# Performance work log

Hardware: AMD Instinct MI355X
Metric: run time of the kernel (lower is better)

Reference implementation:

```python
import jax, jax.numpy as jnp
import numpy as np

N = 4096
S_DIM = 64
A_DIM = 32
HID = 128
HEADS = 4
F = HID // HEADS  # per-head out_features = 32
ALPHA = 0.2       # leaky relu slope
NEG = -9e15       # mask value from the torch code


def _xavier(k, shape, gain=1.0):
    fan_in, fan_out = shape[-2], shape[-1]
    lim = gain * np.sqrt(6.0 / (fan_in + fan_out))
    return jax.random.uniform(k, shape, jnp.float32, -lim, lim)


def setup_inputs() -> dict:
    key = jax.random.key(0)
    ks = jax.random.split(key, 18)
    return {
        "state": jax.random.normal(ks[0], (N, S_DIM), jnp.float32),
        "adj_matrix": jax.random.randint(ks[1], (N, N), 0, 2, jnp.int32),
        # feature extraction MLP
        "W1": _xavier(ks[2], (S_DIM, HID)), "b1": jnp.zeros((HID,), jnp.float32),
        "W2": _xavier(ks[3], (HID, HID)), "b2": jnp.zeros((HID,), jnp.float32),
        # per-head GAT params (stacked over heads); gain=1.414 as in torch init
        "Wg": _xavier(ks[4], (HEADS, HID, F), gain=1.414),
        "ag": _xavier(ks[5], (HEADS, 2 * F, 1), gain=1.414)[..., 0],  # (HEADS, 2F)
        # policy head
        "Wp1": _xavier(ks[6], (HID, HID)), "bp1": jnp.zeros((HID,), jnp.float32),
        "Wp2": _xavier(ks[7], (HID, A_DIM)), "bp2": jnp.zeros((A_DIM,), jnp.float32),
        # value head
        "Wv1": _xavier(ks[8], (HID, HID)), "bv1": jnp.zeros((HID,), jnp.float32),
        "Wv2": _xavier(ks[9], (HID, 1)), "bv2": jnp.zeros((1,), jnp.float32),
    }


def reference(state, adj_matrix, W1, b1, W2, b2, Wg, ag,
              Wp1, bp1, Wp2, bp2, Wv1, bv1, Wv2, bv2):
    # feature extraction MLP: [N, S_DIM] -> [N, HID]
    x = jax.nn.relu(state @ W1 + b1)
    x = jax.nn.relu(x @ W2 + b2)

    # GAT heads (vectorized over heads). h: [H, N, F]
    h = jnp.einsum('nd,hdf->hnf', x, Wg)
    # a^T [h_i || h_j] = a1.h_i + a2.h_j  -> avoid the O(N^2 * 2F) concat
    a1, a2 = ag[:, :F], ag[:, F:]
    s1 = jnp.einsum('hnf,hf->hn', h, a1)  # [H, N]
    s2 = jnp.einsum('hnf,hf->hn', h, a2)  # [H, N]
    e = jax.nn.leaky_relu(s1[:, :, None] + s2[:, None, :], ALPHA)  # [H, N, N]
    mask = adj_matrix > 0
    e = jnp.where(mask[None], e, NEG)
    attn = jax.nn.softmax(e, axis=-1)  # dropout is identity in eval mode
    out = jnp.einsum('hnm,hmf->hnf', attn, h)  # [H, N, F]
    feat = jnp.transpose(out, (1, 0, 2)).reshape(N, HID)  # concat heads along dim=1

    logits = jax.nn.relu(feat @ Wp1 + bp1) @ Wp2 + bp2
    action_probs = jax.nn.softmax(logits, axis=-1)
    state_value = jax.nn.relu(feat @ Wv1 + bv1) @ Wv2 + bv2
    return action_probs, state_value
```

## Files before the change

kernel.cpp:

```cpp
#include <hip/hip_runtime.h>
#include <hip/hip_bf16.h>
#include <hip/hip_fp16.h>

#define NN 4096
#define SDIM 64
#define HID 128
#define HEADS 4
#define FF 32
#define NSPLIT 8

typedef __attribute__((ext_vector_type(8))) _Float16 h8;
typedef __attribute__((ext_vector_type(2))) _Float16 h2;
typedef __attribute__((ext_vector_type(4))) float f32x4;
typedef __attribute__((ext_vector_type(4))) unsigned short us4;


__global__ __launch_bounds__(256) void k_prep_pack(
        const float* __restrict__ state,
        const float* __restrict__ W1, const float* __restrict__ b1,
        const float* __restrict__ W2, const float* __restrict__ b2,
        const float* __restrict__ Wg, const float* __restrict__ ag,
        const int* __restrict__ adj,
        unsigned short* __restrict__ hTf,
        float* __restrict__ s1b, float* __restrict__ s2b,
        unsigned int* __restrict__ abit) {
    int tid = threadIdx.x;

    if (blockIdx.x >= 512) {
        int r = blockIdx.x - 512;
        const int4* ap = (const int4*)(adj + (size_t)r * NN + tid * 16);
        unsigned int b = 0;
#pragma unroll
        for (int i = 0; i < 4; i++) {
            int4 a = ap[i];
            b |= (unsigned int)(a.x != 0) << (i * 4 + 0);
            b |= (unsigned int)(a.y != 0) << (i * 4 + 1);
            b |= (unsigned int)(a.z != 0) << (i * 4 + 2);
            b |= (unsigned int)(a.w != 0) << (i * 4 + 3);
        }
        ((unsigned short*)abit)[r * 256 + tid] = (unsigned short)b;
        return;
    }

    __shared__ float wbuf[8192];
    __shared__ float srow[8][64];
    __shared__ float x1s[8][128];
    __shared__ float x2s[8][128];
    int r0 = blockIdx.x * 8;
    int c = tid & 127, g = tid >> 7;

    if (tid < 128)
        ((float4*)&srow[0][0])[tid] = ((const float4*)(state + (size_t)r0 * SDIM))[tid];
#pragma unroll
    for (int i = 0; i < 8; i++)
        ((float4*)wbuf)[tid + i * 256] = ((const float4*)W1)[tid + i * 256];
    __syncthreads();

    float acc[4];
    {
        float bb = b1[c];
#pragma unroll
        for (int r = 0; r < 4; r++) acc[r] = bb;
#pragma unroll 8
        for (int k = 0; k < SDIM; k++) {
            float w = wbuf[k * HID + c];
#pragma unroll
            for (int r = 0; r < 4; r++) acc[r] += w * srow[g * 4 + r][k];
        }
#pragma unroll
        for (int r = 0; r < 4; r++) x1s[g * 4 + r][c] = fmaxf(acc[r], 0.f);
    }

    {
        float bb = b2[c];
#pragma unroll
        for (int r = 0; r < 4; r++) acc[r] = bb;
#pragma unroll
        for (int hh = 0; hh < 2; hh++) {
            __syncthreads();
#pragma unroll
            for (int i = 0; i < 8; i++)
                ((float4*)wbuf)[tid + i * 256] = ((const float4*)(W2 + hh * 8192))[tid + i * 256];
            __syncthreads();
#pragma unroll 8
            for (int k = 0; k < 64; k++) {
                float w = wbuf[k * HID + c];
#pragma unroll
                for (int r = 0; r < 4; r++) acc[r] += w * x1s[g * 4 + r][hh * 64 + k];
            }
        }
#pragma unroll
        for (int r = 0; r < 4; r++) x2s[g * 4 + r][c] = fmaxf(acc[r], 0.f);
    }

    int hd = c >> 5, f = c & 31;
    float hacc[4];
#pragma unroll
    for (int r = 0; r < 4; r++) hacc[r] = 0.f;
    {
#pragma unroll
        for (int hh = 0; hh < 2; hh++) {
            __syncthreads();
#pragma unroll
            for (int i = 0; i < 32; i++) {
                int L = tid + i * 256;
                int kk = L >> 7, cc = L & 127;
                wbuf[L] = Wg[(cc >> 5) * (HID * FF) + (hh * 64 + kk) * FF + (cc & 31)];
            }
            __syncthreads();
#pragma unroll 8
            for (int k = 0; k < 64; k++) {
                float w = wbuf[k * HID + c];
#pragma unroll
                for (int r = 0; r < 4; r++) hacc[r] += w * x2s[g * 4 + r][hh * 64 + k];
            }
        }
    }

    {
        int bn = f >> 4, fr = f & 15;
        int m31 = (r0 & 31) + g * 4;
        us4 pk;
#pragma unroll
        for (int r = 0; r < 4; r++) pk[r] = __half_as_ushort(__float2half(hacc[r]));
        *(us4*)(hTf + (size_t)((hd * 128 + (r0 >> 5)) * 2 + bn) * 512
                + fr * 32 + (m31 >> 3) * 8 + (m31 & 7)) = pk;
    }

    float a1v = ag[hd * 64 + f];
    float a2v = ag[hd * 64 + 32 + f];
#pragma unroll
    for (int r = 0; r < 4; r++) {
        float p1 = hacc[r] * a1v;
        float p2 = hacc[r] * a2v;
#pragma unroll
        for (int s = 16; s >= 1; s >>= 1) {
            p1 += __shfl_xor(p1, s, 32);
            p2 += __shfl_xor(p2, s, 32);
        }
        if (f == 0) {
            s1b[hd * NN + r0 + g * 4 + r] = p1;
            s2b[hd * NN + r0 + g * 4 + r] = p2;
        }
    }
}

__global__ __launch_bounds__(256, 3) void k_attn(
        const unsigned int* __restrict__ abit, const unsigned short* __restrict__ hTf,
        const float* __restrict__ s1b, const float* __restrict__ s2b,
        __half* __restrict__ pout, float* __restrict__ pden) {
    __shared__ unsigned short hTl[16384];
    __shared__ unsigned int abits[128][17];
    __shared__ unsigned short e2l[512];
    __shared__ unsigned short esl[512];
    __shared__ float redm[4];
    __shared__ uint2 mlut[16];

    int tid = threadIdx.x;
    int tile = blockIdx.x & 31;
    int split = (blockIdx.x >> 5) & 7;
    int hd = blockIdx.x >> 8;
    int nb = tile * 128, m0 = split * 512;

    if (tid < 16) {
        unsigned int lo = ((tid & 1) ? 0xFFFFu : 0u) | ((tid & 2) ? 0xFFFF0000u : 0u);
        unsigned int hi = ((tid & 4) ? 0xFFFFu : 0u) | ((tid & 8) ? 0xFFFF0000u : 0u);
        mlut[tid] = make_uint2(lo, hi);
    }
    {
#pragma unroll
        for (int i = 0; i < 8; i++) {
            int li = tid + i * 256;
            int lane2 = li & 63;
            int fr2 = lane2 & 15, mo2 = lane2 >> 4;
            int ksbn = li >> 6;
            const unsigned short* src = hTf
                + (size_t)((hd * 128 + (m0 >> 5) + (ksbn >> 1)) * 2 + (ksbn & 1)) * 512
                + fr2 * 32 + mo2 * 8;
            *(uint4*)&hTl[li * 8] = *(const uint4*)src;
        }
    }
    {
        int r = tid >> 1, q = (tid & 1) * 8;
        const unsigned int* src = abit + (size_t)(nb + r) * 128 + split * 16 + q;
        *(uint4*)&abits[r][q] = *(const uint4*)src;
        *(uint4*)&abits[r][q + 4] = *(const uint4*)(src + 4);
    }

    {
        float m = -1e30f;
        const f32x4* s2p4 = (const f32x4*)(s2b + hd * NN);
#pragma unroll
        for (int i = 0; i < 4; i++) {
            f32x4 v = s2p4[tid + i * 256];
            m = fmaxf(fmaxf(m, fmaxf(v[0], v[1])), fmaxf(v[2], v[3]));
        }
#pragma unroll
        for (int s = 32; s >= 1; s >>= 1) m = fmaxf(m, __shfl_xor(m, s, 64));
        if ((tid & 63) == 0) redm[tid >> 6] = m;
    }
    __syncthreads();
    float A2 = fmaxf(fmaxf(redm[0], redm[1]), fmaxf(redm[2], redm[3]));

#pragma unroll
    for (int i = 0; i < 2; i++) {
        int mm = tid + i * 256;
        float v2 = s2b[hd * NN + m0 + mm];
        e2l[mm] = __half_as_ushort(__float2half(__expf(v2 - A2)));
        esl[mm] = __half_as_ushort(__float2half(__expf(0.2f * (v2 - A2))));
    }

    int w = tid >> 6, lane = tid & 63;
    int fr = lane & 15, mo = lane >> 4;
    int nw0 = nb + w * 32;

    h2 cph[2], cnh[2];
#pragma unroll
    for (int am = 0; am < 2; am++) {
        int n = nw0 + am * 16 + fr;
        float v1 = s1b[hd * NN + n];
        float u = v1 + A2;
        float C = fmaxf(u, 0.2f * u);
        _Float16 t1 = (_Float16)__expf(u - C);
        _Float16 t2 = (_Float16)__expf(0.2f * u - C);
        cph[am][0] = t1; cph[am][1] = t1;
        cnh[am][0] = t2; cnh[am][1] = t2;
    }
    __syncthreads();

    f32x4 acc[2][2];
    f32x4 accden[2];
#pragma unroll
    for (int am = 0; am < 2; am++) {
#pragma unroll
        for (int bn = 0; bn < 2; bn++) acc[am][bn] = (f32x4){0.f, 0.f, 0.f, 0.f};
        accden[am] = (f32x4){0.f, 0.f, 0.f, 0.f};
    }

    h8 ones;
#pragma unroll
    for (int j = 0; j < 8; j++) ones[j] = (_Float16)1.0f;

#pragma unroll 2
    for (int ks = 0; ks < 16; ks++) {
        h8 B0 = *(const h8*)&hTl[(ks * 2 + 0) * 512 + lane * 8];
        h8 B1 = *(const h8*)&hTl[(ks * 2 + 1) * 512 + lane * 8];
        const h2* e2p = (const h2*)&e2l[ks * 32 + mo * 8];
        const h2* esp = (const h2*)&esl[ks * 32 + mo * 8];

#pragma unroll
        for (int am = 0; am < 2; am++) {
            unsigned int bits = abits[w * 32 + am * 16 + fr][ks] >> (mo * 8);
            uint2 m01 = mlut[bits & 15];
            uint2 m23 = mlut[(bits >> 4) & 15];
            union { unsigned int u[4]; h8 v; } A;
#pragma unroll
            for (int p = 0; p < 4; p++) {
                h2 w2 = __builtin_elementwise_max(cph[am] * e2p[p], cnh[am] * esp[p]);
                unsigned int wm;
                __builtin_memcpy(&wm, &w2, 4);
                unsigned int mk = (p == 0) ? m01.x : (p == 1) ? m01.y : (p == 2) ? m23.x : m23.y;
                A.u[p] = wm & mk;
            }
            acc[am][0] = __builtin_amdgcn_mfma_f32_16x16x32_f16(A.v, B0, acc[am][0], 0, 0, 0);
            acc[am][1] = __builtin_amdgcn_mfma_f32_16x16x32_f16(A.v, B1, acc[am][1], 0, 0, 0);
            accden[am] = __builtin_amdgcn_mfma_f32_16x16x32_f16(A.v, ones, accden[am], 0, 0, 0);
        }
    }

    __half* pob = pout + ((size_t)(split * 4 + hd) * NN + nw0) * FF;
#pragma unroll
    for (int am = 0; am < 2; am++) {
#pragma unroll
        for (int bn = 0; bn < 2; bn++) {
            f32x4 cv = acc[am][bn];
#pragma unroll
            for (int r = 0; r < 4; r++)
                pob[(am * 16 + mo * 4 + r) * FF + bn * 16 + fr] = __float2half(cv[r]);
        }
        if (fr == 0) {
#pragma unroll
            for (int r = 0; r < 4; r++)
                pden[(size_t)(split * 4 + hd) * NN + nw0 + am * 16 + mo * 4 + r] = accden[am][r];
        }
    }
}

__global__ __launch_bounds__(512) void k_redpolval(
        const __half* __restrict__ pout, const float* __restrict__ pden,
        const float* __restrict__ Wp1, const float* __restrict__ bp1,
        const float* __restrict__ Wp2, const float* __restrict__ bp2,
        const float* __restrict__ Wv1, const float* __restrict__ bv1,
        const float* __restrict__ Wv2, const float* __restrict__ bv2,
        float* __restrict__ out) {
    __shared__ float fr[16][128];
    __shared__ float hh[16][128];
    __shared__ float dens[16][4];
    int tid = threadIdx.x;
    int r0 = blockIdx.x * 16;

    {
        int p = tid >> 3, sg = tid & 7;
        int r = p >> 2, hd = p & 3;
        float d = pden[(size_t)(sg * 4 + hd) * NN + r0 + r];
#pragma unroll
        for (int s = 4; s >= 1; s >>= 1) d += __shfl_xor(d, s, 8);
        if (sg == 0) dens[r][hd] = d;
    }

    int row = tid >> 5, c4 = (tid & 31) * 4;
    int hd2 = c4 >> 5;
    float o4[4] = {0.f, 0.f, 0.f, 0.f};
    const __half* pp = pout + ((size_t)hd2 * NN + r0 + row) * 32 + (c4 & 31);
#pragma unroll
    for (int s = 0; s < NSPLIT; s++) {
        float2 raw = *(const float2*)(pp + (size_t)s * 4 * NN * 32);
        __half2 ha = *(__half2*)&raw.x;
        __half2 hb = *(__half2*)&raw.y;
        float2 fa = __half22float2(ha), fb = __half22float2(hb);
        o4[0] += fa.x; o4[1] += fa.y; o4[2] += fb.x; o4[3] += fb.y;
    }
    __syncthreads();
    {
        float dn = fmaxf(dens[row][hd2], 1e-30f);
#pragma unroll
        for (int i = 0; i < 4; i++) fr[row][c4 + i] = o4[i] / dn;
    }
    __syncthreads();

    int c = tid & 127, g = tid >> 7;
    int c2 = tid & 31, r = tid >> 5;

    {
        float acc[4];
        float bb = bp1[c];
#pragma unroll
        for (int q = 0; q < 4; q++) acc[q] = bb;
#pragma unroll 8
        for (int k = 0; k < HID; k++) {
            float w = Wp1[k * HID + c];
#pragma unroll
            for (int q = 0; q < 4; q++) acc[q] += w * fr[g * 4 + q][k];
        }
#pragma unroll
        for (int q = 0; q < 4; q++) hh[g * 4 + q][c] = fmaxf(acc[q], 0.f);
    }
    __syncthreads();
    {
        float lacc = bp2[c2];
#pragma unroll 8
        for (int k = 0; k < HID; k++) lacc += hh[r][k] * Wp2[k * 32 + c2];
        float mx = lacc;
#pragma unroll
        for (int s = 16; s >= 1; s >>= 1) mx = fmaxf(mx, __shfl_xor(mx, s, 32));
        float e = __expf(lacc - mx);
        float sm = e;
#pragma unroll
        for (int s = 16; s >= 1; s >>= 1) sm += __shfl_xor(sm, s, 32);
        out[(size_t)(r0 + r) * 32 + c2] = e / sm;
    }
    __syncthreads();

    {
        float acc[4];
        float bb = bv1[c];
#pragma unroll
        for (int q = 0; q < 4; q++) acc[q] = bb;
#pragma unroll 8
        for (int k = 0; k < HID; k++) {
            float w = Wv1[k * HID + c];
#pragma unroll
            for (int q = 0; q < 4; q++) acc[q] += w * fr[g * 4 + q][k];
        }
#pragma unroll
        for (int q = 0; q < 4; q++) hh[g * 4 + q][c] = fmaxf(acc[q], 0.f);
    }
    __syncthreads();
    {
        float p = 0.f;
#pragma unroll
        for (int j = 0; j < 4; j++) p += hh[r][c2 + j * 32] * Wv2[c2 + j * 32];
#pragma unroll
        for (int s = 16; s >= 1; s >>= 1) p += __shfl_xor(p, s, 32);
        if (c2 == 0) out[131072 + r0 + r] = p + bv2[0];
    }
}

extern "C" void kernel_launch(void* const* d_in, const int* in_sizes, int n_in,
                              void* d_out, int out_size, void* d_ws, size_t ws_size,
                              hipStream_t stream) {
    const float* state = (const float*)d_in[0];
    const int*   adj   = (const int*)d_in[1];
    const float* W1  = (const float*)d_in[2];
    const float* b1  = (const float*)d_in[3];
    const float* W2  = (const float*)d_in[4];
    const float* b2  = (const float*)d_in[5];
    const float* Wg  = (const float*)d_in[6];
    const float* ag  = (const float*)d_in[7];
    const float* Wp1 = (const float*)d_in[8];
    const float* bp1 = (const float*)d_in[9];
    const float* Wp2 = (const float*)d_in[10];
    const float* bp2 = (const float*)d_in[11];
    const float* Wv1 = (const float*)d_in[12];
    const float* bv1 = (const float*)d_in[13];
    const float* Wv2 = (const float*)d_in[14];
    const float* bv2 = (const float*)d_in[15];
    float* out = (float*)d_out;
    float* ws = (float*)d_ws;

    unsigned short* hTf = (unsigned short*)ws;
    float* s1b  = ws + 262144;
    float* s2b  = ws + 278528;
    unsigned int* abit = (unsigned int*)(ws + 294912);
    __half* pout = (__half*)(ws + 819200);
    float* pden = ws + 2916352;

    hipLaunchKernelGGL(k_prep_pack, dim3(512 + NN), dim3(256), 0, stream,
                       state, W1, b1, W2, b2, Wg, ag, adj, hTf, s1b, s2b, abit);
    hipLaunchKernelGGL(k_attn, dim3(32 * NSPLIT * HEADS), dim3(256), 0, stream,
                       abit, hTf, s1b, s2b, pout, pden);
    hipLaunchKernelGGL(k_redpolval, dim3(NN / 16), dim3(512), 0, stream,
                       pout, pden, Wp1, bp1, Wp2, bp2, Wv1, bv1, Wv2, bv2, out);
}
```

Measured before the change: 55.13 us.

## Fuse three kernels into one cooperative persistent kernel with grid syncs

Merges the prep/pack, attention and reduction/policy-value kernels into a single cooperative kernel of 512 blocks separated by grid.sync, with each block looping over several attention work items. The attention split count doubles to 16 so each block handles 256 key columns per item, and the final reduction sums more partials. The goal is to remove launch gaps and tail effects between kernels. In exchange it adds grid-wide barrier cost, lower per-phase parallelism (prep work now spread over 512 blocks instead of 4608), extra partial-sum traffic, and host-side occupancy queries on every call.

Result: no change. 54.78 us (-0.6%).

```diff
diff --git a/kernel.cpp b/kernel.cpp
--- a/kernel.cpp
+++ b/kernel.cpp
@@ -1,5 +1,5 @@
 #include <hip/hip_runtime.h>
-#include <hip/hip_bf16.h>
+#include <hip/hip_cooperative_groups.h>
 #include <hip/hip_fp16.h>
 
 #define NN 4096
@@ -7,13 +7,394 @@
 #define HID 128
 #define HEADS 4
 #define FF 32
-#define NSPLIT 8
+#define NSPLIT 16
+#define NSPLIT_FB 8
 
 typedef __attribute__((ext_vector_type(8))) _Float16 h8;
 typedef __attribute__((ext_vector_type(2))) _Float16 h2;
 typedef __attribute__((ext_vector_type(4))) float f32x4;
 typedef __attribute__((ext_vector_type(4))) unsigned short us4;
 
+
+__global__ __launch_bounds__(256, 2) void k_fused(
+        const float* __restrict__ state,
+        const float* __restrict__ W1, const float* __restrict__ b1,
+        const float* __restrict__ W2, const float* __restrict__ b2,
+        const float* __restrict__ Wg, const float* __restrict__ ag,
+        const int* __restrict__ adj,
+        const float* __restrict__ Wp1, const float* __restrict__ bp1,
+        const float* __restrict__ Wp2, const float* __restrict__ bp2,
+        const float* __restrict__ Wv1, const float* __restrict__ bv1,
+        const float* __restrict__ Wv2, const float* __restrict__ bv2,
+        unsigned short* __restrict__ hTf,
+        float* __restrict__ s1b, float* __restrict__ s2b,
+        unsigned int* __restrict__ abit,
+        __half* __restrict__ pout, float* __restrict__ pden,
+        float* __restrict__ out) {
+    __shared__ __align__(16) unsigned char smem[26624];
+    cooperative_groups::grid_group grid = cooperative_groups::this_grid();
+    int tid = threadIdx.x;
+    int bid = blockIdx.x;
+
+    if (bid >= 256) {
+        int rb = (bid - 256) * 16;
+#pragma unroll
+        for (int rr = 0; rr < 16; rr++) {
+            const int4* ap = (const int4*)(adj + (size_t)(rb + rr) * NN + tid * 16);
+            unsigned int b = 0;
+#pragma unroll
+            for (int i = 0; i < 4; i++) {
+                int4 a = ap[i];
+                b |= (unsigned int)(a.x != 0) << (i * 4 + 0);
+                b |= (unsigned int)(a.y != 0) << (i * 4 + 1);
+                b |= (unsigned int)(a.z != 0) << (i * 4 + 2);
+                b |= (unsigned int)(a.w != 0) << (i * 4 + 3);
+            }
+            ((unsigned short*)abit)[(rb + rr) * 256 + tid] = (unsigned short)b;
+        }
+    } else {
+        float* wbuf = (float*)smem;
+        float (*srow)[64] = (float(*)[64])(smem + 16384);
+        float (*x1s)[128] = (float(*)[128])(smem + 18432);
+        float (*x2s)[128] = (float(*)[128])(smem + 22528);
+        int c = tid & 127, g = tid >> 7;
+
+        for (int uu = 0; uu < 2; uu++) {
+            int r0 = (bid * 2 + uu) * 8;
+            if (tid < 128)
+                ((float4*)&srow[0][0])[tid] = ((const float4*)(state + (size_t)r0 * SDIM))[tid];
+
+            float acc[4];
+            {
+                float bb = b1[c];
+#pragma unroll
+                for (int r = 0; r < 4; r++) acc[r] = bb;
+#pragma unroll
+                for (int q = 0; q < 2; q++) {
+                    __syncthreads();
+#pragma unroll
+                    for (int i = 0; i < 4; i++)
+                        ((float4*)wbuf)[tid + i * 256] = ((const float4*)(W1 + q * 4096))[tid + i * 256];
+                    __syncthreads();
+#pragma unroll 8
+                    for (int k = 0; k < 32; k++) {
+                        float w = wbuf[k * HID + c];
+#pragma unroll
+                        for (int r = 0; r < 4; r++) acc[r] += w * srow[g * 4 + r][q * 32 + k];
+                    }
+                }
+#pragma unroll
+                for (int r = 0; r < 4; r++) x1s[g * 4 + r][c] = fmaxf(acc[r], 0.f);
+            }
+            {
+                float bb = b2[c];
+#pragma unroll
+                for (int r = 0; r < 4; r++) acc[r] = bb;
+#pragma unroll
+                for (int q = 0; q < 4; q++) {
+                    __syncthreads();
+#pragma unroll
+                    for (int i = 0; i < 4; i++)
+                        ((float4*)wbuf)[tid + i * 256] = ((const float4*)(W2 + q * 4096))[tid + i * 256];
+                    __syncthreads();
+#pragma unroll 8
+                    for (int k = 0; k < 32; k++) {
+                        float w = wbuf[k * HID + c];
+#pragma unroll
+                        for (int r = 0; r < 4; r++) acc[r] += w * x1s[g * 4 + r][q * 32 + k];
+                    }
+                }
+#pragma unroll
+                for (int r = 0; r < 4; r++) x2s[g * 4 + r][c] = fmaxf(acc[r], 0.f);
+            }
+            int hd = c >> 5, f = c & 31;
+            float hacc[4];
+#pragma unroll
+            for (int r = 0; r < 4; r++) hacc[r] = 0.f;
+            {
+#pragma unroll
+                for (int q = 0; q < 4; q++) {
+                    __syncthreads();
+#pragma unroll
+                    for (int i = 0; i < 16; i++) {
+                        int L = tid + i * 256;
+                        int kk = L >> 7, cc = L & 127;
+                        wbuf[L] = Wg[(cc >> 5) * (HID * FF) + (q * 32 + kk) * FF + (cc & 31)];
+                    }
+                    __syncthreads();
+#pragma unroll 8
+                    for (int k = 0; k < 32; k++) {
+                        float w = wbuf[k * HID + c];
+#pragma unroll
+                        for (int r = 0; r < 4; r++) hacc[r] += w * x2s[g * 4 + r][q * 32 + k];
+                    }
+                }
+            }
+            {
+                int bn = f >> 4, fr = f & 15;
+                int m31 = (r0 & 31) + g * 4;
+                us4 pk;
+#pragma unroll
+                for (int r = 0; r < 4; r++) pk[r] = __half_as_ushort(__float2half(hacc[r]));
+                *(us4*)(hTf + (size_t)((hd * 128 + (r0 >> 5)) * 2 + bn) * 512
+                        + fr * 32 + (m31 >> 3) * 8 + (m31 & 7)) = pk;
+            }
+            float a1v = ag[hd * 64 + f];
+            float a2v = ag[hd * 64 + 32 + f];
+#pragma unroll
+            for (int r = 0; r < 4; r++) {
+                float p1 = hacc[r] * a1v;
+                float p2 = hacc[r] * a2v;
+#pragma unroll
+                for (int s = 16; s >= 1; s >>= 1) {
+                    p1 += __shfl_xor(p1, s, 32);
+                    p2 += __shfl_xor(p2, s, 32);
+                }
+                if (f == 0) {
+                    s1b[hd * NN + r0 + g * 4 + r] = p1;
+                    s2b[hd * NN + r0 + g * 4 + r] = p2;
+                }
+            }
+        }
+    }
+    __threadfence();
+    grid.sync();
+
+    {
+        unsigned short* hTl = (unsigned short*)smem;
+        unsigned int (*abits)[9] = (unsigned int(*)[9])(smem + 16384);
+        unsigned short* e2l = (unsigned short*)(smem + 20992);
+        unsigned short* esl = (unsigned short*)(smem + 21504);
+        float* redm = (float*)(smem + 22016);
+        uint2* mlut = (uint2*)(smem + 22032);
+
+#pragma unroll 1
+        for (int t = 0; t < 4; t++) {
+            __syncthreads();
+            int work = bid + t * 512;
+            int tile = work & 31;
+            int split = (work >> 5) & 15;
+            int hd = work >> 9;
+            int nb = tile * 128, m0 = split * 256;
+
+            if (tid < 16) {
+                unsigned int lo = ((tid & 1) ? 0xFFFFu : 0u) | ((tid & 2) ? 0xFFFF0000u : 0u);
+                unsigned int hi = ((tid & 4) ? 0xFFFFu : 0u) | ((tid & 8) ? 0xFFFF0000u : 0u);
+                mlut[tid] = make_uint2(lo, hi);
+            }
+            {
+#pragma unroll
+                for (int i = 0; i < 4; i++) {
+                    int li = tid + i * 256;
+                    int lane2 = li & 63;
+                    int fr2 = lane2 & 15, mo2 = lane2 >> 4;
+                    int ksbn = li >> 6;
+                    const unsigned short* src = hTf
+                        + (size_t)((hd * 128 + (m0 >> 5) + (ksbn >> 1)) * 2 + (ksbn & 1)) * 512
+                        + fr2 * 32 + mo2 * 8;
+                    *(uint4*)&hTl[li * 8] = *(const uint4*)src;
+                }
+            }
+            {
+                int r = tid >> 1, q = (tid & 1) * 4;
+                const unsigned int* src = abit + (size_t)(nb + r) * 128 + split * 8 + q;
+                *(uint4*)&abits[r][q] = *(const uint4*)src;
+            }
+            {
+                float m = -1e30f;
+                const f32x4* s2p4 = (const f32x4*)(s2b + hd * NN);
+#pragma unroll
+                for (int i = 0; i < 4; i++) {
+                    f32x4 v = s2p4[tid + i * 256];
+                    m = fmaxf(fmaxf(m, fmaxf(v[0], v[1])), fmaxf(v[2], v[3]));
+                }
+#pragma unroll
+                for (int s = 32; s >= 1; s >>= 1) m = fmaxf(m, __shfl_xor(m, s, 64));
+                if ((tid & 63) == 0) redm[tid >> 6] = m;
+            }
+            __syncthreads();
+            float A2 = fmaxf(fmaxf(redm[0], redm[1]), fmaxf(redm[2], redm[3]));
+
+            {
+                float v2 = s2b[hd * NN + m0 + tid];
+                e2l[tid] = __half_as_ushort(__float2half(__expf(v2 - A2)));
+                esl[tid] = __half_as_ushort(__float2half(__expf(0.2f * (v2 - A2))));
+            }
+
+            int w = tid >> 6, lane = tid & 63;
+            int fr = lane & 15, mo = lane >> 4;
+            int nw0 = nb + w * 32;
+
+            h2 cph[2], cnh[2];
+#pragma unroll
+            for (int am = 0; am < 2; am++) {
+                int n = nw0 + am * 16 + fr;
+                float v1 = s1b[hd * NN + n];
+                float u = v1 + A2;
+                float C = fmaxf(u, 0.2f * u);
+                _Float16 t1 = (_Float16)__expf(u - C);
+                _Float16 t2 = (_Float16)__expf(0.2f * u - C);
+                cph[am][0] = t1; cph[am][1] = t1;
+                cnh[am][0] = t2; cnh[am][1] = t2;
+            }
+            __syncthreads();
+
+            f32x4 acc[2][2];
+            f32x4 accden[2];
+#pragma unroll
+            for (int am = 0; am < 2; am++) {
+#pragma unroll
+                for (int bn = 0; bn < 2; bn++) acc[am][bn] = (f32x4){0.f, 0.f, 0.f, 0.f};
+                accden[am] = (f32x4){0.f, 0.f, 0.f, 0.f};
+            }
+            h8 ones;
+#pragma unroll
+            for (int j = 0; j < 8; j++) ones[j] = (_Float16)1.0f;
+
+#pragma unroll 2
+            for (int ks = 0; ks < 8; ks++) {
+                h8 B0 = *(const h8*)&hTl[(ks * 2 + 0) * 512 + lane * 8];
+                h8 B1 = *(const h8*)&hTl[(ks * 2 + 1) * 512 + lane * 8];
+                const h2* e2p = (const h2*)&e2l[ks * 32 + mo * 8];
+                const h2* esp = (const h2*)&esl[ks * 32 + mo * 8];
+
+#pragma unroll
+                for (int am = 0; am < 2; am++) {
+                    unsigned int bits = abits[w * 32 + am * 16 + fr][ks] >> (mo * 8);
+                    uint2 m01 = mlut[bits & 15];
+                    uint2 m23 = mlut[(bits >> 4) & 15];
+                    union { unsigned int u[4]; h8 v; } A;
+#pragma unroll
+                    for (int p = 0; p < 4; p++) {
+                        h2 w2 = __builtin_elementwise_max(cph[am] * e2p[p], cnh[am] * esp[p]);
+                        unsigned int wm;
+                        __builtin_memcpy(&wm, &w2, 4);
+                        unsigned int mk = (p == 0) ? m01.x : (p == 1) ? m01.y : (p == 2) ? m23.x : m23.y;
+                        A.u[p] = wm & mk;
+                    }
+                    acc[am][0] = __builtin_amdgcn_mfma_f32_16x16x32_f16(A.v, B0, acc[am][0], 0, 0, 0);
+                    acc[am][1] = __builtin_amdgcn_mfma_f32_16x16x32_f16(A.v, B1, acc[am][1], 0, 0, 0);
+                    accden[am] = __builtin_amdgcn_mfma_f32_16x16x32_f16(A.v, ones, accden[am], 0, 0, 0);
+                }
+            }
+
+            __half* pob = pout + ((size_t)(split * 4 + hd) * NN + nw0) * FF;
+#pragma unroll
+            for (int am = 0; am < 2; am++) {
+#pragma unroll
+                for (int bn = 0; bn < 2; bn++) {
+                    f32x4 cv = acc[am][bn];
+#pragma unroll
+                    for (int r = 0; r < 4; r++)
+                        pob[(am * 16 + mo * 4 + r) * FF + bn * 16 + fr] = __float2half(cv[r]);
+                }
+                if (fr == 0) {
+#pragma unroll
+                    for (int r = 0; r < 4; r++)
+                        pden[(size_t)(split * 4 + hd) * NN + nw0 + am * 16 + mo * 4 + r] = accden[am][r];
+                }
+            }
+        }
+    }
+    __threadfence();
+    grid.sync();
+
+    {
+        float (*fr8)[128] = (float(*)[128])smem;
+        float (*hh)[128] = (float(*)[128])(smem + 4096);
+        float (*dens)[4] = (float(*)[4])(smem + 8192);
+        int r0 = bid * 8;
+        __syncthreads();
+
+        {
+            int p = tid >> 3, sg = tid & 7;
+            int r = p >> 2, hd = p & 3;
+            float d = 0.f;
+#pragma unroll
+            for (int i = 0; i < 2; i++)
+                d += pden[(size_t)((sg + i * 8) * 4 + hd) * NN + r0 + r];
+#pragma unroll
+            for (int s = 4; s >= 1; s >>= 1) d += __shfl_xor(d, s, 8);
+            if (sg == 0) dens[r][hd] = d;
+        }
+
+        int row = tid >> 5, c4 = (tid & 31) * 4;
+        int hd2 = c4 >> 5;
+        float o4[4] = {0.f, 0.f, 0.f, 0.f};
+        const __half* pp = pout + ((size_t)hd2 * NN + r0 + row) * 32 + (c4 & 31);
+#pragma unroll
+        for (int s = 0; s < NSPLIT; s++) {
+            float2 raw = *(const float2*)(pp + (size_t)s * 4 * NN * 32);
+            __half2 ha = *(__half2*)&raw.x;
+            __half2 hb = *(__half2*)&raw.y;
+            float2 fa = __half22float2(ha), fb = __half22float2(hb);
+            o4[0] += fa.x; o4[1] += fa.y; o4[2] += fb.x; o4[3] += fb.y;
+        }
+        __syncthreads();
+        {
+            float dn = fmaxf(dens[row][hd2], 1e-30f);
+#pragma unroll
+            for (int i = 0; i < 4; i++) fr8[row][c4 + i] = o4[i] / dn;
+        }
+        __syncthreads();
+
+        int c = tid & 127, g = tid >> 7;
+        int c2 = tid & 31, r = tid >> 5;
+
+        {
+            float acc[4];
+            float bb = bp1[c];
+#pragma unroll
+            for (int q = 0; q < 4; q++) acc[q] = bb;
+#pragma unroll 8
+            for (int k = 0; k < HID; k++) {
+                float w = Wp1[k * HID + c];
+#pragma unroll
+                for (int q = 0; q < 4; q++) acc[q] += w * fr8[g * 4 + q][k];
+            }
+#pragma unroll
+            for (int q = 0; q < 4; q++) hh[g * 4 + q][c] = fmaxf(acc[q], 0.f);
+        }
+        __syncthreads();
+        {
+            float lacc = bp2[c2];
+#pragma unroll 8
+            for (int k = 0; k < HID; k++) lacc += hh[r][k] * Wp2[k * 32 + c2];
+            float mx = lacc;
+#pragma unroll
+            for (int s = 16; s >= 1; s >>= 1) mx = fmaxf(mx, __shfl_xor(mx, s, 32));
+            float e = __expf(lacc - mx);
+            float sm = e;
+#pragma unroll
+            for (int s = 16; s >= 1; s >>= 1) sm += __shfl_xor(sm, s, 32);
+            out[(size_t)(r0 + r) * 32 + c2] = e / sm;
+        }
+        __syncthreads();
+        {
+            float acc[4];
+            float bb = bv1[c];
+#pragma unroll
+            for (int q = 0; q < 4; q++) acc[q] = bb;
+#pragma unroll 8
+            for (int k = 0; k < HID; k++) {
+                float w = Wv1[k * HID + c];
+#pragma unroll
+                for (int q = 0; q < 4; q++) acc[q] += w * fr8[g * 4 + q][k];
+            }
+#pragma unroll
+            for (int q = 0; q < 4; q++) hh[g * 4 + q][c] = fmaxf(acc[q], 0.f);
+        }
+        __syncthreads();
+        {
+            float p = 0.f;
+#pragma unroll
+            for (int j = 0; j < 4; j++) p += hh[r][c2 + j * 32] * Wv2[c2 + j * 32];
+#pragma unroll
+            for (int s = 16; s >= 1; s >>= 1) p += __shfl_xor(p, s, 32);
+            if (c2 == 0) out[131072 + r0 + r] = p + bv2[0];
+        }
+    }
+}
 
 __global__ __launch_bounds__(256) void k_prep_pack(
         const float* __restrict__ state,
@@ -70,7 +451,6 @@
 #pragma unroll
         for (int r = 0; r < 4; r++) x1s[g * 4 + r][c] = fmaxf(acc[r], 0.f);
     }
-
     {
         float bb = b2[c];
 #pragma unroll
@@ -92,7 +472,6 @@
 #pragma unroll
         for (int r = 0; r < 4; r++) x2s[g * 4 + r][c] = fmaxf(acc[r], 0.f);
     }
-
     int hd = c >> 5, f = c & 31;
     float hacc[4];
 #pragma unroll
@@ -116,7 +495,6 @@
             }
         }
     }
-
     {
         int bn = f >> 4, fr = f & 15;
         int m31 = (r0 & 31) + g * 4;
@@ -126,7 +504,6 @@
         *(us4*)(hTf + (size_t)((hd * 128 + (r0 >> 5)) * 2 + bn) * 512
                 + fr * 32 + (m31 >> 3) * 8 + (m31 & 7)) = pk;
     }
-
     float a1v = ag[hd * 64 + f];
     float a2v = ag[hd * 64 + 32 + f];
 #pragma unroll
@@ -145,7 +522,7 @@
     }
 }
 
-__global__ __launch_bounds__(256, 3) void k_attn(
+__global__ __launch_bounds__(256, 3) void k_attn_fb(
         const unsigned int* __restrict__ abit, const unsigned short* __restrict__ hTf,
         const float* __restrict__ s1b, const float* __restrict__ s2b,
         __half* __restrict__ pout, float* __restrict__ pden) {
@@ -186,7 +563,6 @@
         *(uint4*)&abits[r][q] = *(const uint4*)src;
         *(uint4*)&abits[r][q + 4] = *(const uint4*)(src + 4);
     }
-
     {
         float m = -1e30f;
         const f32x4* s2p4 = (const f32x4*)(s2b + hd * NN);
@@ -236,7 +612,6 @@
         for (int bn = 0; bn < 2; bn++) acc[am][bn] = (f32x4){0.f, 0.f, 0.f, 0.f};
         accden[am] = (f32x4){0.f, 0.f, 0.f, 0.f};
     }
-
     h8 ones;
 #pragma unroll
     for (int j = 0; j < 8; j++) ones[j] = (_Float16)1.0f;
@@ -286,14 +661,14 @@
     }
 }
 
-__global__ __launch_bounds__(512) void k_redpolval(
+__global__ __launch_bounds__(512) void k_redpolval_fb(
         const __half* __restrict__ pout, const float* __restrict__ pden,
         const float* __restrict__ Wp1, const float* __restrict__ bp1,
         const float* __restrict__ Wp2, const float* __restrict__ bp2,
         const float* __restrict__ Wv1, const float* __restrict__ bv1,
         const float* __restrict__ Wv2, const float* __restrict__ bv2,
         float* __restrict__ out) {
-    __shared__ float fr[16][128];
+    __shared__ float fr8[16][128];
     __shared__ float hh[16][128];
     __shared__ float dens[16][4];
     int tid = threadIdx.x;
@@ -313,7 +688,7 @@
     float o4[4] = {0.f, 0.f, 0.f, 0.f};
     const __half* pp = pout + ((size_t)hd2 * NN + r0 + row) * 32 + (c4 & 31);
 #pragma unroll
-    for (int s = 0; s < NSPLIT; s++) {
+    for (int s = 0; s < NSPLIT_FB; s++) {
         float2 raw = *(const float2*)(pp + (size_t)s * 4 * NN * 32);
         __half2 ha = *(__half2*)&raw.x;
         __half2 hb = *(__half2*)&raw.y;
@@ -324,7 +699,7 @@
     {
         float dn = fmaxf(dens[row][hd2], 1e-30f);
 #pragma unroll
-        for (int i = 0; i < 4; i++) fr[row][c4 + i] = o4[i] / dn;
+        for (int i = 0; i < 4; i++) fr8[row][c4 + i] = o4[i] / dn;
     }
     __syncthreads();
 
@@ -340,7 +715,7 @@
         for (int k = 0; k < HID; k++) {
             float w = Wp1[k * HID + c];
 #pragma unroll
-            for (int q = 0; q < 4; q++) acc[q] += w * fr[g * 4 + q][k];
+            for (int q = 0; q < 4; q++) acc[q] += w * fr8[g * 4 + q][k];
         }
 #pragma unroll
         for (int q = 0; q < 4; q++) hh[g * 4 + q][c] = fmaxf(acc[q], 0.f);
@@ -360,7 +735,6 @@
         out[(size_t)(r0 + r) * 32 + c2] = e / sm;
     }
     __syncthreads();
-
     {
         float acc[4];
         float bb = bv1[c];
@@ -370,7 +744,7 @@
         for (int k = 0; k < HID; k++) {
             float w = Wv1[k * HID + c];
 #pragma unroll
-            for (int q = 0; q < 4; q++) acc[q] += w * fr[g * 4 + q][k];
+            for (int q = 0; q < 4; q++) acc[q] += w * fr8[g * 4 + q][k];
         }
 #pragma unroll
         for (int q = 0; q < 4; q++) hh[g * 4 + q][c] = fmaxf(acc[q], 0.f);
@@ -413,12 +787,31 @@
     float* s2b  = ws + 278528;
     unsigned int* abit = (unsigned int*)(ws + 294912);
     __half* pout = (__half*)(ws + 819200);
-    float* pden = ws + 2916352;
+    float* pden = ws + 5013504;
+
+    int dev = 0;
+    hipGetDevice(&dev);
+    int nCU = 0;
+    hipDeviceGetAttribute(&nCU, hipDeviceAttributeMultiprocessorCount, dev);
+    int maxB = 0;
+    hipError_t qe = hipOccupancyMaxActiveBlocksPerMultiprocessor(&maxB, k_fused, 256, 0);
+
+    if (qe == hipSuccess && (long)maxB * nCU >= 512) {
+        void* args[] = { (void*)&state, (void*)&W1, (void*)&b1, (void*)&W2, (void*)&b2,
+                         (void*)&Wg, (void*)&ag, (void*)&adj,
+                         (void*)&Wp1, (void*)&bp1, (void*)&Wp2, (void*)&bp2,
+                         (void*)&Wv1, (void*)&bv1, (void*)&Wv2, (void*)&bv2,
+                         (void*)&hTf, (void*)&s1b, (void*)&s2b, (void*)&abit,
+                         (void*)&pout, (void*)&pden, (void*)&out };
+        hipError_t le = hipLaunchCooperativeKernel((void*)k_fused, dim3(512), dim3(256),
+                                                   args, 0, stream);
+        if (le == hipSuccess) return;
+    }
 
     hipLaunchKernelGGL(k_prep_pack, dim3(512 + NN), dim3(256), 0, stream,
                        state, W1, b1, W2, b2, Wg, ag, adj, hTf, s1b, s2b, abit);
-    hipLaunchKernelGGL(k_attn, dim3(32 * NSPLIT * HEADS), dim3(256), 0, stream,
+    hipLaunchKernelGGL(k_attn_fb, dim3(32 * NSPLIT_FB * HEADS), dim3(256), 0, stream,
                        abit, hTf, s1b, s2b, pout, pden);
-    hipLaunchKernelGGL(k_redpolval, dim3(NN / 16), dim3(512), 0, stream,
+    hipLaunchKernelGGL(k_redpolval_fb, dim3(NN / 16), dim3(512), 0, stream,
                        pout, pden, Wp1, bp1, Wp2, bp2, Wv1, bv1, Wv2, bv2, out);
 }
```
